# Kernel optimization log

Measured on AMD Instinct MI355X. Metric: run time of the kernel, lower is better.

Reference implementation:

```python
import jax, jax.numpy as jnp
import numpy as np
from jax import lax

N, D, H = 4096, 768, 16384


def setup_inputs() -> dict:
    key = jax.random.key(0)
    k0, k1, k2, k3, k4, k5, k6 = jax.random.split(key, 7)
    bound_e = 1.0 / np.sqrt(D)   # kaiming_uniform(a=sqrt(5)) on (H, D) -> bound 1/sqrt(fan_in)
    bound_d = 1.0 / np.sqrt(H)   # nn.Linear default init, fan_in = H
    return {
        "vision_embeddings": jax.random.normal(k0, (N, D), dtype=jnp.float32),
        "text_embeddings": jax.random.normal(k1, (N, D), dtype=jnp.float32),
        "encoder": jax.random.uniform(k2, (H, D), jnp.float32, -bound_e, bound_e),
        "Wv": jax.random.uniform(k3, (D, H), jnp.float32, -bound_d, bound_d),
        "bv": jax.random.uniform(k4, (D,), jnp.float32, -bound_d, bound_d),
        "Wt": jax.random.uniform(k5, (D, H), jnp.float32, -bound_d, bound_d),
        "bt": jax.random.uniform(k6, (D,), jnp.float32, -bound_d, bound_d),
        "topk": 32,
    }


def _l2norm(x, axis):
    return x / jnp.maximum(jnp.linalg.norm(x, axis=axis, keepdims=True), 1e-12)


def _encode(emb, encoder, topk):
    # F.normalize rows, then cdist(p=2) between unit vectors: ||a-b|| = sqrt(2-2 a.b)
    w = _l2norm(encoder, axis=1)            # [H, D]
    e = _l2norm(emb, axis=1)                # [N, D]
    cos = jnp.einsum("nd,hd->nh", e, w)     # [N, H]
    dist = jnp.sqrt(jnp.maximum(2.0 - 2.0 * cos, 0.0))
    sim = 2.0 - dist                         # [N, H]
    # kthvalue(abs, k=H-topk) == (topk+1)-th largest; keep strictly-greater entries
    abs_f = jnp.abs(sim)
    thres = lax.top_k(abs_f, topk + 1)[0][:, -1]  # [N]
    mask = (abs_f > thres[:, None]).astype(sim.dtype)
    return sim * mask


def reference(vision_embeddings, text_embeddings, encoder, Wv, bv, Wt, bt, topk):
    latent_v = _encode(vision_embeddings, encoder, topk)          # [N, H]
    recon_v = jnp.einsum("nh,dh->nd", latent_v, Wv) + bv          # [N, D]
    latent_t = _encode(text_embeddings, encoder, topk)            # [N, H]
    recon_t = jnp.einsum("nh,dh->nd", latent_t, Wt) + bt          # [N, D]
    return (recon_v, recon_t, latent_v, latent_t)
```

## Files before the change

### kernel.cpp

```cpp
#include <hip/hip_runtime.h>
#include <math.h>


#define N_ROWS 4096
#define D_DIM  768
#define H_DIM  16384
#define M_TOT  8192
#define TOPK   32
#define MARGIN 1e-3f
#define SEL_CAP 40
#define AMB_CAP 64
#define CCAP   512
#define SCAP   24
#define THR_COS 0.08f
#define THR_SIM_GUARD 0.6436f

typedef __attribute__((ext_vector_type(8))) short short8;
typedef __attribute__((ext_vector_type(4))) float floatx4;

__device__ inline unsigned short bf16_rne(float f) {
    unsigned u = __float_as_uint(f);
    unsigned r = u + 0x7fffu + ((u >> 16) & 1u);
    return (unsigned short)(r >> 16);
}

__device__ inline void gload16(const unsigned short* g, unsigned short* l) {
    __builtin_amdgcn_global_load_lds(
        (const __attribute__((address_space(1))) void*)g,
        (__attribute__((address_space(3))) void*)l, 16, 0, 0);
}

__global__ void split_all_kernel(const float* __restrict__ embv,
                                 const float* __restrict__ embt,
                                 const float* __restrict__ enc,
                                 unsigned short* __restrict__ Ahi,
                                 unsigned short* __restrict__ Alo,
                                 unsigned short* __restrict__ Bh,
                                 float* __restrict__ invA,
                                 float* __restrict__ invB,
                                 int* __restrict__ cntflag)
{
    int row = blockIdx.x;
    int tid = threadIdx.x;
    if (row < 64) {
        cntflag[row * 256 + tid] = 0;
    }
    const float* src;
    unsigned short *hi, *lo;
    float* invp;
    if (row < N_ROWS) {
        src = embv + (size_t)row * D_DIM;
        hi = Ahi + (size_t)row * D_DIM; lo = Alo + (size_t)row * D_DIM;
        invp = invA + row;
    } else if (row < 2 * N_ROWS) {
        int r = row - N_ROWS;
        src = embt + (size_t)r * D_DIM;
        hi = Ahi + (size_t)row * D_DIM; lo = Alo + (size_t)row * D_DIM;
        invp = invA + row;
    } else {
        int r = row - 2 * N_ROWS;
        src = enc + (size_t)r * D_DIM;
        hi = Bh + (size_t)r * D_DIM; lo = nullptr;
        invp = invB + r;
    }
    __shared__ float red[4];
    const float4* s4 = reinterpret_cast<const float4*>(src);
    float4 v = make_float4(0.f, 0.f, 0.f, 0.f);
    float ss = 0.f;
    if (tid < 192) {
        v = s4[tid];
        ss = v.x * v.x + v.y * v.y + v.z * v.z + v.w * v.w;
    }
    #pragma unroll
    for (int o = 32; o > 0; o >>= 1) ss += __shfl_down(ss, o);
    int wave = tid >> 6, lane = tid & 63;
    if (lane == 0) red[wave] = ss;
    __syncthreads();
    if (tid == 0) {
        float tot = red[0] + red[1] + red[2];
        red[0] = 1.f / fmaxf(sqrtf(tot), 1e-12f);
    }
    __syncthreads();
    float inv = red[0];
    if (tid == 0) *invp = inv;
    if (tid < 192) {
        float x[4] = {v.x * inv, v.y * inv, v.z * inv, v.w * inv};
        unsigned short hh[4], ll[4];
        #pragma unroll
        for (int t = 0; t < 4; t++) {
            hh[t] = bf16_rne(x[t]);
            float hf = __uint_as_float((unsigned)hh[t] << 16);
            ll[t] = bf16_rne(x[t] - hf);
        }
        ushort4 h4; h4.x = hh[0]; h4.y = hh[1]; h4.z = hh[2]; h4.w = hh[3];
        *reinterpret_cast<ushort4*>(hi + tid * 4) = h4;
        if (lo) {
            ushort4 l4; l4.x = ll[0]; l4.y = ll[1]; l4.z = ll[2]; l4.w = ll[3];
            *reinterpret_cast<ushort4*>(lo + tid * 4) = l4;
        }
    }
}

#define GBK 32
#define NTILE (D_DIM / GBK)

__global__ __launch_bounds__(256, 3)
void gemm_mfma_kernel(const unsigned short* __restrict__ Ahi,
                      const unsigned short* __restrict__ Alo,
                      const unsigned short* __restrict__ Bh,
                      int* __restrict__ cand_cnt,
                      int* __restrict__ cand_idx,
                      float* __restrict__ cand_val)
{
    __shared__ unsigned short sA[2][2][128 * GBK];
    __shared__ unsigned short sB[2][128 * GBK];

    int tid = threadIdx.x;
    int lane = tid & 63;
    int wave = tid >> 6;
    int wr = (wave >> 1) * 64;
    int wc = (wave & 1) * 64;
    int m = lane & 15;
    int q = lane >> 4;

    unsigned nwgx = gridDim.x;
    unsigned lid = blockIdx.y * nwgx + blockIdx.x;
    unsigned cpx = (nwgx * gridDim.y) >> 3;
    unsigned swz = (lid & 7u) * cpx + (lid >> 3);
    int bx = (int)(swz % nwgx);
    int by = (int)(swz / nwgx);

    int row0 = by * 128;
    int col0 = bx * 128;

    int p0 = tid, p1 = tid + 256;
    int r0 = ((p0 >> 5) << 3) | (p0 & 7), q0 = (p0 >> 3) & 3;
    int r1 = ((p1 >> 5) << 3) | (p1 & 7), q1 = (p1 >> 3) & 3;
    size_t aoff0 = (size_t)(row0 + r0) * D_DIM + q0 * 8;
    size_t aoff1 = (size_t)(row0 + r1) * D_DIM + q1 * 8;
    size_t boff0 = (size_t)(col0 + r0) * D_DIM + q0 * 8;
    size_t boff1 = (size_t)(col0 + r1) * D_DIM + q1 * 8;

    int am0 = wr + m;
    int bn0 = wc + m;
    int offA = ((am0 >> 3) << 8) + (q << 6) + ((am0 & 7) << 3);
    int offB = ((bn0 >> 3) << 8) + (q << 6) + ((bn0 & 7) << 3);

    floatx4 acc[4][4];
    #pragma unroll
    for (int i = 0; i < 4; i++)
        #pragma unroll
        for (int j = 0; j < 4; j++)
            acc[i][j] = (floatx4){0.f, 0.f, 0.f, 0.f};

    auto stage = [&](int t, int b) {
        int k0 = t * GBK;
        gload16(Ahi + aoff0 + k0, &sA[b][0][p0 * 8]);
        gload16(Ahi + aoff1 + k0, &sA[b][0][p1 * 8]);
        gload16(Alo + aoff0 + k0, &sA[b][1][p0 * 8]);
        gload16(Alo + aoff1 + k0, &sA[b][1][p1 * 8]);
        gload16(Bh + boff0 + k0, &sB[b][p0 * 8]);
        gload16(Bh + boff1 + k0, &sB[b][p1 * 8]);
    };

    auto compute = [&](int b) {
        short8 fah[4], fal[4], fbv[4];
        #pragma unroll
        for (int i = 0; i < 4; i++) {
            fah[i] = *(const short8*)&sA[b][0][offA + i * 512];
            fal[i] = *(const short8*)&sA[b][1][offA + i * 512];
        }
        #pragma unroll
        for (int j = 0; j < 4; j++)
            fbv[j] = *(const short8*)&sB[b][offB + j * 512];
        __builtin_amdgcn_s_setprio(1);
        #pragma unroll
        for (int j = 0; j < 4; j++) {
            #pragma unroll
            for (int i = 0; i < 4; i++) {
                acc[i][j] = __builtin_amdgcn_mfma_f32_16x16x32_bf16(fah[i], fbv[j], acc[i][j], 0, 0, 0);
                acc[i][j] = __builtin_amdgcn_mfma_f32_16x16x32_bf16(fal[i], fbv[j], acc[i][j], 0, 0, 0);
            }
        }
        __builtin_amdgcn_s_setprio(0);
    };

    stage(0, 0);
    int cur = 0;
    for (int t = 0; t < NTILE - 1; ++t) {
        stage(t + 1, cur ^ 1);
        asm volatile("s_waitcnt vmcnt(6)" ::: "memory");
        __builtin_amdgcn_s_barrier();
        __builtin_amdgcn_sched_barrier(0);
        compute(cur);
        __builtin_amdgcn_sched_barrier(0);
        __builtin_amdgcn_s_barrier();
        cur ^= 1;
    }
    asm volatile("s_waitcnt vmcnt(0)" ::: "memory");
    __builtin_amdgcn_s_barrier();
    __builtin_amdgcn_sched_barrier(0);
    compute(cur);

    __syncthreads();
    int*   s_rcnt = (int*)(&sA[0][0][0]);
    int*   s_ridx = s_rcnt + 128;
    float* s_rval = (float*)(s_ridx + 128 * SCAP);
    if (tid < 128) s_rcnt[tid] = 0;
    __syncthreads();

    #pragma unroll
    for (int i = 0; i < 4; i++) {
        #pragma unroll
        for (int r = 0; r < 4; r++) {
            int lrow = wr + i * 16 + q * 4 + r;
            #pragma unroll
            for (int j = 0; j < 4; j++) {
                float cosv = acc[i][j][r];
                if (cosv >= THR_COS) {
                    int s = atomicAdd(&s_rcnt[lrow], 1);
                    if (s < SCAP) {
                        s_ridx[lrow * SCAP + s] = wc + m + j * 16;
                        s_rval[lrow * SCAP + s] = cosv;
                    }
                }
            }
        }
    }
    __syncthreads();

    if (tid < 128) {
        int c = s_rcnt[tid];
        if (c > 0) {
            int grow = row0 + tid;
            int wcnt = (c > SCAP) ? SCAP : c;
            int addc = (c > SCAP) ? (CCAP + 1) : c;
            int base = atomicAdd(&cand_cnt[grow], addc);
            for (int s2 = 0; s2 < wcnt; ++s2) {
                int slot = base + s2;
                if (slot < CCAP) {
                    cand_idx[(size_t)grow * CCAP + slot] = col0 + s_ridx[tid * SCAP + s2];
                    cand_val[(size_t)grow * CCAP + slot] = s_rval[tid * SCAP + s2];
                }
            }
        }
    }
}

__global__ __launch_bounds__(256)
void cand_select_kernel(const int* __restrict__ cand_cnt,
                        const int* __restrict__ cand_idx,
                        const float* __restrict__ cand_val,
                        float* __restrict__ latent,
                        int* __restrict__ sel_cnt,
                        int* __restrict__ sel_idx,
                        float* __restrict__ sel_val,
                        int* __restrict__ amb_cnt,
                        int* __restrict__ amb_idx,
                        int* __restrict__ flag)
{
    int row = blockIdx.x;
    int tid = threadIdx.x;
    float* v = latent + (size_t)row * H_DIM;

    floatx4* vw = (floatx4*)v;
    floatx4 z = (floatx4){0.f, 0.f, 0.f, 0.f};
    #pragma unroll
    for (int k = 0; k < 16; k++)
        __builtin_nontemporal_store(z, &vw[tid + 256 * k]);

    int cnt = cand_cnt[row];

    __shared__ float sv[CCAP];
    __shared__ int   si[CCAP];
    __shared__ int svstar, skept, samb;

    if (cnt > CCAP || cnt < TOPK + 1) {
        if (tid == 0) { flag[row] = 1; sel_cnt[row] = 0; amb_cnt[row] = 0; }
        return;
    }
    for (int c = tid; c < cnt; c += 256) {
        float cosv = cand_val[(size_t)row * CCAP + c];
        sv[c] = 2.f - sqrtf(fmaxf(2.f - 2.f * cosv, 0.f));
        si[c] = cand_idx[(size_t)row * CCAP + c];
    }
    if (tid == 0) { svstar = 0x7FFFFFFF; skept = 0; samb = 0; }
    __syncthreads();

    for (int c = tid; c < cnt; c += 256) {
        float a = sv[c];
        int g = 0;
        for (int j = 0; j < cnt; j++) {
            float aj = sv[j];
            g += (aj > a || (aj == a && j < c)) ? 1 : 0;
        }
        if (g <= TOPK) atomicMin(&svstar, __float_as_int(a));
    }
    __syncthreads();
    float vs = __int_as_float(svstar);

    if (vs - MARGIN <= THR_SIM_GUARD) {
        if (tid == 0) { flag[row] = 1; sel_cnt[row] = 0; amb_cnt[row] = 0; }
        return;
    }

    for (int c = tid; c < cnt; c += 256) {
        float f = sv[c];
        int idx = si[c];
        if (f > vs + MARGIN) {
            int s = atomicAdd(&skept, 1);
            sel_idx[(size_t)row * SEL_CAP + s] = idx;
            sel_val[(size_t)row * SEL_CAP + s] = f;
            v[idx] = f;
        } else if (f >= vs - MARGIN) {
            int s = atomicAdd(&samb, 1);
            if (s < AMB_CAP) amb_idx[(size_t)row * AMB_CAP + s] = idx;
        }
    }
    __syncthreads();
    if (tid == 0) { sel_cnt[row] = skept; amb_cnt[row] = min(samb, AMB_CAP); }
}

__global__ __launch_bounds__(256)
void finalize_kernel(const int* __restrict__ flag,
                     const float* __restrict__ embv,
                     const float* __restrict__ embt,
                     const float* __restrict__ enc,
                     const float* __restrict__ invA,
                     const float* __restrict__ invB,
                     float* __restrict__ latent,
                     int* __restrict__ sel_cnt,
                     int* __restrict__ sel_idx,
                     float* __restrict__ sel_val,
                     int* __restrict__ amb_cnt,
                     const int* __restrict__ amb_idx)
{
    int row = blockIdx.x;
    int tid = threadIdx.x;
    float* v = latent + (size_t)row * H_DIM;
    const float* src = (row < N_ROWS) ? embv + (size_t)row * D_DIM
                                      : embt + (size_t)(row - N_ROWS) * D_DIM;
    float ia = invA[row];

    __shared__ float ssrc[D_DIM];
    __shared__ unsigned hist[256];
    __shared__ unsigned s_prefix;
    __shared__ int s_k, s_cnt;
    __shared__ float ex[AMB_CAP];
    __shared__ int evs, kc;

    if (flag[row]) {
        for (int d = tid; d < D_DIM; d += 256) ssrc[d] = src[d];
        __syncthreads();
        for (int h = tid; h < H_DIM; h += 256) {
            const float* w = enc + (size_t)h * D_DIM;
            float d = 0.f;
            for (int t = 0; t < D_DIM; t++) d += ssrc[t] * w[t];
            float cosv = d * ia * invB[h];
            v[h] = 2.f - sqrtf(fmaxf(2.f - 2.f * cosv, 0.f));
        }
        __syncthreads();
        int k = TOPK + 1;
        unsigned prefix = 0;
        for (int shift = 24; shift >= 0; shift -= 8) {
            hist[tid] = 0;
            __syncthreads();
            unsigned pmask = (shift == 24) ? 0u : (0xFFFFFFFFu << (shift + 8));
            for (int i = tid; i < H_DIM; i += 256) {
                unsigned u = __float_as_uint(v[i]);
                if ((u & pmask) == prefix)
                    atomicAdd(&hist[(u >> shift) & 255u], 1u);
            }
            __syncthreads();
            if (tid == 0) {
                int c = 0, b = 255;
                for (; b >= 0; b--) {
                    c += (int)hist[b];
                    if (c >= k) break;
                }
                if (b < 0) b = 0;
                s_prefix = prefix | ((unsigned)b << shift);
                s_k = k - (c - (int)hist[b]);
            }
            __syncthreads();
            prefix = s_prefix;
            k = s_k;
            __syncthreads();
        }
        float thres = __uint_as_float(prefix);
        if (tid == 0) s_cnt = 0;
        __syncthreads();
        for (int i = tid; i < H_DIM; i += 256) {
            float x = v[i];
            bool keep = (x > thres);
            v[i] = keep ? x : 0.f;
            if (keep) {
                int slot = atomicAdd(&s_cnt, 1);
                if (slot < SEL_CAP) {
                    sel_idx[(size_t)row * SEL_CAP + slot] = i;
                    sel_val[(size_t)row * SEL_CAP + slot] = x;
                }
            }
        }
        __syncthreads();
        if (tid == 0) {
            sel_cnt[row] = (s_cnt > SEL_CAP) ? SEL_CAP : s_cnt;
            amb_cnt[row] = 0;
        }
        return;
    }

    int s = amb_cnt[row];
    if (s == 0) return;
    int m = sel_cnt[row];
    int need = TOPK - m;
    if (need <= 0) return;
    int wave = tid >> 6, lane = tid & 63;
    for (int a = wave; a < s; a += 4) {
        int h = amb_idx[(size_t)row * AMB_CAP + a];
        const float* w = enc + (size_t)h * D_DIM;
        float d = 0.f;
        for (int t = lane; t < D_DIM; t += 64) d += src[t] * w[t];
        #pragma unroll
        for (int o = 32; o > 0; o >>= 1) d += __shfl_down(d, o);
        if (lane == 0) {
            float cosv = d * ia * invB[h];
            ex[a] = 2.f - sqrtf(fmaxf(2.f - 2.f * cosv, 0.f));
        }
    }
    if (tid == 0) { evs = 0x7FFFFFFF; kc = 0; }
    __syncthreads();
    if (tid < s) {
        float mya = fabsf(ex[tid]);
        int g = 0;
        for (int j = 0; j < s; j++) {
            float aj = fabsf(ex[j]);
            g += (aj > mya || (aj == mya && j < tid)) ? 1 : 0;
        }
        if (g <= need) atomicMin(&evs, __float_as_int(mya));
    }
    __syncthreads();
    float ep = __int_as_float(evs);
    if (tid < s) {
        int idx = amb_idx[(size_t)row * AMB_CAP + tid];
        float e = ex[tid];
        if (fabsf(e) > ep) {
            int sl = atomicAdd(&kc, 1);
            v[idx] = e;
            sel_idx[(size_t)row * SEL_CAP + m + sl] = idx;
            sel_val[(size_t)row * SEL_CAP + m + sl] = e;
        }
    }
    __syncthreads();
    if (tid == 0) sel_cnt[row] = m + kc;
}

__global__ void transpose_kernel(const float* __restrict__ Wv,
                                 const float* __restrict__ Wt,
                                 float* __restrict__ WvT,
                                 float* __restrict__ WtT)
{
    int z = blockIdx.z;
    const float* W = z ? Wt : Wv;
    float* WT = z ? WtT : WvT;
    __shared__ float tile[32][33];
    int tx = threadIdx.x & 31;
    int ty = threadIdx.x >> 5;
    int h0 = blockIdx.x * 32;
    int d0 = blockIdx.y * 32;
    #pragma unroll
    for (int t = 0; t < 4; t++)
        tile[ty + t * 8][tx] = W[(size_t)(d0 + ty + t * 8) * H_DIM + h0 + tx];
    __syncthreads();
    #pragma unroll
    for (int t = 0; t < 4; t++)
        WT[(size_t)(h0 + ty + t * 8) * D_DIM + d0 + tx] = tile[tx][ty + t * 8];
}

__global__ void recon_kernel(const float* __restrict__ Wv_,
                             const float* __restrict__ Wt_,
                             const float* __restrict__ bv,
                             const float* __restrict__ bt,
                             const int* __restrict__ sel_cnt,
                             const int* __restrict__ sel_idx,
                             const float* __restrict__ sel_val,
                             long sh, long sd,
                             float* __restrict__ out)
{
    int n = blockIdx.x;
    int z = blockIdx.y;
    int row = z * N_ROWS + n;
    const float* W = z ? Wt_ : Wv_;
    const float* bias = z ? bt : bv;
    float* o = out + (size_t)z * N_ROWS * D_DIM + (size_t)n * D_DIM;

    __shared__ int s_idx[SEL_CAP];
    __shared__ float s_val[SEL_CAP];
    __shared__ int s_cnt;
    int tid = threadIdx.x;
    if (tid == 0) s_cnt = sel_cnt[row];
    __syncthreads();
    int cnt = s_cnt;
    if (tid < cnt) {
        s_idx[tid] = sel_idx[(size_t)row * SEL_CAP + tid];
        s_val[tid] = sel_val[(size_t)row * SEL_CAP + tid];
    }
    __syncthreads();

    for (int d = tid; d < D_DIM; d += 256) {
        float acc = bias[d];
        for (int j = 0; j < cnt; j++)
            acc += s_val[j] * W[(size_t)s_idx[j] * sh + (size_t)d * sd];
        o[d] = acc;
    }
}

__global__ void row_invnorm_kernel(const float* __restrict__ x,
                                   float* __restrict__ inv, int rows) {
    int row = blockIdx.x * 4 + (threadIdx.x >> 6);
    int lane = threadIdx.x & 63;
    if (row >= rows) return;
    const float4* p = reinterpret_cast<const float4*>(x + (size_t)row * D_DIM);
    float ss = 0.f;
    #pragma unroll
    for (int i = 0; i < 3; i++) {
        float4 v = p[lane + i * 64];
        ss += v.x * v.x + v.y * v.y + v.z * v.z + v.w * v.w;
    }
    #pragma unroll
    for (int off = 32; off > 0; off >>= 1) ss += __shfl_down(ss, off);
    if (lane == 0) inv[row] = 1.f / fmaxf(sqrtf(ss), 1e-12f);
}

#define BM 128
#define BN 128
#define BK 16
__global__ __launch_bounds__(256)
void gemm_sim_kernel(const float* __restrict__ embv,
                     const float* __restrict__ embt,
                     const float* __restrict__ enc,
                     const float* __restrict__ inv_emb,
                     const float* __restrict__ inv_enc,
                     float* __restrict__ latent)
{
    int z = blockIdx.z;
    const float* A = z ? embt : embv;
    const float* invA = inv_emb + z * N_ROWS;
    float* C = latent + (size_t)z * N_ROWS * H_DIM;
    __shared__ float As[BK][BM + 4];
    __shared__ float Bs[BK][BN + 4];
    int tid = threadIdx.x;
    int tx = tid & 15, ty = tid >> 4;
    int row0 = blockIdx.y * BM, col0 = blockIdx.x * BN;
    float acc[8][8];
    #pragma unroll
    for (int i = 0; i < 8; i++)
        #pragma unroll
        for (int j = 0; j < 8; j++) acc[i][j] = 0.f;
    for (int k0 = 0; k0 < D_DIM; k0 += BK) {
        #pragma unroll
        for (int t = 0; t < 2; t++) {
            int idx = t * 256 + tid;
            int r = idx >> 2, c4 = idx & 3;
            float4 va = *reinterpret_cast<const float4*>(
                A + (size_t)(row0 + r) * D_DIM + k0 + c4 * 4);
            As[c4 * 4 + 0][r] = va.x; As[c4 * 4 + 1][r] = va.y;
            As[c4 * 4 + 2][r] = va.z; As[c4 * 4 + 3][r] = va.w;
            float4 vb = *reinterpret_cast<const float4*>(
                enc + (size_t)(col0 + r) * D_DIM + k0 + c4 * 4);
            Bs[c4 * 4 + 0][r] = vb.x; Bs[c4 * 4 + 1][r] = vb.y;
            Bs[c4 * 4 + 2][r] = vb.z; Bs[c4 * 4 + 3][r] = vb.w;
        }
        __syncthreads();
        #pragma unroll
        for (int kk = 0; kk < BK; kk++) {
            float a[8], b[8];
            *reinterpret_cast<float4*>(&a[0]) = *reinterpret_cast<const float4*>(&As[kk][ty * 8]);
            *reinterpret_cast<float4*>(&a[4]) = *reinterpret_cast<const float4*>(&As[kk][ty * 8 + 4]);
            *reinterpret_cast<float4*>(&b[0]) = *reinterpret_cast<const float4*>(&Bs[kk][tx * 8]);
            *reinterpret_cast<float4*>(&b[4]) = *reinterpret_cast<const float4*>(&Bs[kk][tx * 8 + 4]);
            #pragma unroll
            for (int i = 0; i < 8; i++)
                #pragma unroll
                for (int j = 0; j < 8; j++)
                    acc[i][j] = fmaf(a[i], b[j], acc[i][j]);
        }
        __syncthreads();
    }
    #pragma unroll
    for (int i = 0; i < 8; i++) {
        int n = row0 + ty * 8 + i;
        float sa = invA[n];
        float* Crow = C + (size_t)n * H_DIM + col0 + tx * 8;
        float tmp[8];
        #pragma unroll
        for (int j = 0; j < 8; j++) {
            float cosv = acc[i][j] * sa * inv_enc[col0 + tx * 8 + j];
            tmp[j] = 2.f - sqrtf(fmaxf(2.f - 2.f * cosv, 0.f));
        }
        float4 o0 = {tmp[0], tmp[1], tmp[2], tmp[3]};
        float4 o1 = {tmp[4], tmp[5], tmp[6], tmp[7]};
        *reinterpret_cast<float4*>(Crow) = o0;
        *reinterpret_cast<float4*>(Crow + 4) = o1;
    }
}

__global__ void legacy_select_kernel(float* __restrict__ latent,
                                     const int* __restrict__ topk_p,
                                     int* __restrict__ sel_cnt,
                                     int* __restrict__ sel_idx,
                                     float* __restrict__ sel_val)
{
    int row = blockIdx.x;
    float* v = latent + (size_t)row * H_DIM;
    int tid = threadIdx.x;
    __shared__ unsigned hist[256];
    __shared__ unsigned s_prefix;
    __shared__ int s_k;
    __shared__ int s_cnt;
    int k = topk_p[0] + 1;
    unsigned prefix = 0;
    for (int shift = 24; shift >= 0; shift -= 8) {
        hist[tid] = 0;
        __syncthreads();
        unsigned pmask = (shift == 24) ? 0u : (0xFFFFFFFFu << (shift + 8));
        for (int i = tid; i < H_DIM; i += 256) {
            unsigned u = __float_as_uint(v[i]) & 0x7FFFFFFFu;
            if ((u & pmask) == prefix)
                atomicAdd(&hist[(u >> shift) & 255u], 1u);
        }
        __syncthreads();
        if (tid == 0) {
            int c = 0, b = 255;
            for (; b >= 0; b--) {
                c += (int)hist[b];
                if (c >= k) break;
            }
            if (b < 0) b = 0;
            s_prefix = prefix | ((unsigned)b << shift);
            s_k = k - (c - (int)hist[b]);
        }
        __syncthreads();
        prefix = s_prefix;
        k = s_k;
        __syncthreads();
    }
    float thres = __uint_as_float(prefix);
    if (tid == 0) s_cnt = 0;
    __syncthreads();
    for (int i = tid; i < H_DIM; i += 256) {
        float x = v[i];
        bool keep = (fabsf(x) > thres);
        v[i] = keep ? x : 0.f;
        if (keep) {
            int slot = atomicAdd(&s_cnt, 1);
            if (slot < SEL_CAP) {
                sel_idx[(size_t)row * SEL_CAP + slot] = i;
                sel_val[(size_t)row * SEL_CAP + slot] = x;
            }
        }
    }
    __syncthreads();
    if (tid == 0) sel_cnt[row] = (s_cnt > SEL_CAP) ? SEL_CAP : s_cnt;
}

extern "C" void kernel_launch(void* const* d_in, const int* in_sizes, int n_in,
                              void* d_out, int out_size, void* d_ws, size_t ws_size,
                              hipStream_t stream) {
    const float* embv = (const float*)d_in[0];
    const float* embt = (const float*)d_in[1];
    const float* enc  = (const float*)d_in[2];
    const float* Wv   = (const float*)d_in[3];
    const float* bv   = (const float*)d_in[4];
    const float* Wt   = (const float*)d_in[5];
    const float* bt   = (const float*)d_in[6];
    const int* topk   = (const int*)d_in[7];
    float* out = (float*)d_out;

    float* recon_out = out;
    float* latent = out + (size_t)2 * N_ROWS * D_DIM;

    char* ws = (char*)d_ws;
    size_t off = 0;
    float* invA = (float*)(ws + off);            off += (size_t)M_TOT * 4;
    float* invB = (float*)(ws + off);            off += (size_t)H_DIM * 4;
    int*   sel_cnt = (int*)(ws + off);           off += (size_t)M_TOT * 4;
    int*   amb_cnt = (int*)(ws + off);           off += (size_t)M_TOT * 4;
    int*   sel_idx = (int*)(ws + off);           off += (size_t)M_TOT * SEL_CAP * 4;
    float* sel_val = (float*)(ws + off);         off += (size_t)M_TOT * SEL_CAP * 4;
    int*   amb_idx = (int*)(ws + off);           off += (size_t)M_TOT * AMB_CAP * 4;
    int*   cand_cnt = (int*)(ws + off);          off += (size_t)M_TOT * 4;
    int*   flag     = (int*)(ws + off);          off += (size_t)M_TOT * 4;
    unsigned short* Ahi = (unsigned short*)(ws + off); off += (size_t)M_TOT * D_DIM * 2;
    unsigned short* Alo = (unsigned short*)(ws + off); off += (size_t)M_TOT * D_DIM * 2;
    unsigned short* Bh  = (unsigned short*)(ws + off); off += (size_t)H_DIM * D_DIM * 2;
    size_t core_need = off;

    int*   cand_idx = (int*)(ws + off);
    float* cand_val = (float*)(ws + off + (size_t)M_TOT * CCAP * 4);
    size_t cand_bytes = (size_t)M_TOT * CCAP * 8;
    float* WvT = (float*)(ws + off);
    float* WtT = WvT + (size_t)D_DIM * H_DIM;
    size_t trans_bytes = (size_t)2 * D_DIM * H_DIM * 4;

    if (ws_size >= core_need + cand_bytes) {
        bool use_T = ws_size >= core_need + trans_bytes;

        split_all_kernel<<<2 * N_ROWS + H_DIM, 256, 0, stream>>>(
            embv, embt, enc, Ahi, Alo, Bh, invA, invB, cand_cnt);

        gemm_mfma_kernel<<<dim3(H_DIM / 128, M_TOT / 128), 256, 0, stream>>>(
            Ahi, Alo, Bh, cand_cnt, cand_idx, cand_val);

        cand_select_kernel<<<M_TOT, 256, 0, stream>>>(
            cand_cnt, cand_idx, cand_val, latent,
            sel_cnt, sel_idx, sel_val, amb_cnt, amb_idx, flag);

        finalize_kernel<<<M_TOT, 256, 0, stream>>>(
            flag, embv, embt, enc, invA, invB, latent,
            sel_cnt, sel_idx, sel_val, amb_cnt, amb_idx);

        if (use_T) {
            transpose_kernel<<<dim3(H_DIM / 32, D_DIM / 32, 2), 256, 0, stream>>>(
                Wv, Wt, WvT, WtT);
            recon_kernel<<<dim3(N_ROWS, 2), 256, 0, stream>>>(
                WvT, WtT, bv, bt, sel_cnt, sel_idx, sel_val, (long)D_DIM, 1L, recon_out);
        } else {
            recon_kernel<<<dim3(N_ROWS, 2), 256, 0, stream>>>(
                Wv, Wt, bv, bt, sel_cnt, sel_idx, sel_val, 1L, (long)H_DIM, recon_out);
        }
    } else {
        size_t o2 = 0;
        float* inv_enc = (float*)(ws + o2); o2 += (size_t)H_DIM * 4;
        float* inv_emb = (float*)(ws + o2); o2 += (size_t)2 * N_ROWS * 4;
        int*   l_cnt = (int*)(ws + o2);     o2 += (size_t)2 * N_ROWS * 4;
        int*   l_idx = (int*)(ws + o2);     o2 += (size_t)2 * N_ROWS * SEL_CAP * 4;
        float* l_val = (float*)(ws + o2);   o2 += (size_t)2 * N_ROWS * SEL_CAP * 4;
        row_invnorm_kernel<<<H_DIM / 4, 256, 0, stream>>>(enc, inv_enc, H_DIM);
        row_invnorm_kernel<<<N_ROWS / 4, 256, 0, stream>>>(embv, inv_emb, N_ROWS);
        row_invnorm_kernel<<<N_ROWS / 4, 256, 0, stream>>>(embt, inv_emb + N_ROWS, N_ROWS);
        dim3 g(H_DIM / BN, N_ROWS / BM, 2);
        gemm_sim_kernel<<<g, 256, 0, stream>>>(embv, embt, enc, inv_emb, inv_enc, latent);
        legacy_select_kernel<<<2 * N_ROWS, 256, 0, stream>>>(latent, topk, l_cnt, l_idx, l_val);
        recon_kernel<<<dim3(N_ROWS, 2), 256, 0, stream>>>(
            Wv, Wt, bv, bt, l_cnt, l_idx, l_val, 1L, (long)H_DIM, recon_out);
    }
}
```

Measured before the change: 1.454 ms.

## Fuse candidate selection with finalize and add vectorized float4 recon kernel

Merges the candidate-select and finalize kernels into one per-row kernel, so ambiguous indices stay in shared memory and the flag, amb_cnt and amb_idx round trips through global memory plus one launch are removed. The fallback dot product now uses float4 loads. Reconstruction uses a new 192-thread kernel where each thread accumulates a float4 slice of the transposed weights. The host also drops the non-transposed path and requires workspace for the transposed weights. Fusing the two kernels may raise shared-memory use and register pressure in the combined kernel.

```diff
diff --git a/kernel.cpp b/kernel.cpp
--- a/kernel.cpp
+++ b/kernel.cpp
@@ -248,16 +248,18 @@
 }
 
 __global__ __launch_bounds__(256)
-void cand_select_kernel(const int* __restrict__ cand_cnt,
-                        const int* __restrict__ cand_idx,
-                        const float* __restrict__ cand_val,
-                        float* __restrict__ latent,
-                        int* __restrict__ sel_cnt,
-                        int* __restrict__ sel_idx,
-                        float* __restrict__ sel_val,
-                        int* __restrict__ amb_cnt,
-                        int* __restrict__ amb_idx,
-                        int* __restrict__ flag)
+void select_finalize_kernel(const int* __restrict__ cand_cnt,
+                            const int* __restrict__ cand_idx,
+                            const float* __restrict__ cand_val,
+                            const float* __restrict__ embv,
+                            const float* __restrict__ embt,
+                            const float* __restrict__ enc,
+                            const float* __restrict__ invA,
+                            const float* __restrict__ invB,
+                            float* __restrict__ latent,
+                            int* __restrict__ sel_cnt,
+                            int* __restrict__ sel_idx,
+                            float* __restrict__ sel_val)
 {
     int row = blockIdx.x;
     int tid = threadIdx.x;
@@ -273,34 +275,100 @@
 
     __shared__ float sv[CCAP];
     __shared__ int   si[CCAP];
-    __shared__ int svstar, skept, samb;
-
-    if (cnt > CCAP || cnt < TOPK + 1) {
-        if (tid == 0) { flag[row] = 1; sel_cnt[row] = 0; amb_cnt[row] = 0; }
-        return;
-    }
-    for (int c = tid; c < cnt; c += 256) {
-        float cosv = cand_val[(size_t)row * CCAP + c];
-        sv[c] = 2.f - sqrtf(fmaxf(2.f - 2.f * cosv, 0.f));
-        si[c] = cand_idx[(size_t)row * CCAP + c];
-    }
-    if (tid == 0) { svstar = 0x7FFFFFFF; skept = 0; samb = 0; }
-    __syncthreads();
-
-    for (int c = tid; c < cnt; c += 256) {
-        float a = sv[c];
-        int g = 0;
-        for (int j = 0; j < cnt; j++) {
-            float aj = sv[j];
-            g += (aj > a || (aj == a && j < c)) ? 1 : 0;
-        }
-        if (g <= TOPK) atomicMin(&svstar, __float_as_int(a));
-    }
-    __syncthreads();
-    float vs = __int_as_float(svstar);
-
-    if (vs - MARGIN <= THR_SIM_GUARD) {
-        if (tid == 0) { flag[row] = 1; sel_cnt[row] = 0; amb_cnt[row] = 0; }
+    __shared__ int   s_amb[AMB_CAP];
+    __shared__ float ex[AMB_CAP];
+    __shared__ float ssrc[D_DIM];
+    __shared__ unsigned hist[256];
+    __shared__ unsigned s_prefix;
+    __shared__ int svstar, skept, samb, s_k, s_cnt2, evs, kc;
+
+    bool bad = (cnt > CCAP || cnt < TOPK + 1);
+    float vs = 0.f;
+    if (!bad) {
+        for (int c = tid; c < cnt; c += 256) {
+            float cosv = cand_val[(size_t)row * CCAP + c];
+            sv[c] = 2.f - sqrtf(fmaxf(2.f - 2.f * cosv, 0.f));
+            si[c] = cand_idx[(size_t)row * CCAP + c];
+        }
+        if (tid == 0) { svstar = 0x7FFFFFFF; skept = 0; samb = 0; }
+        __syncthreads();
+        for (int c = tid; c < cnt; c += 256) {
+            float a = sv[c];
+            int g = 0;
+            for (int j = 0; j < cnt; j++) {
+                float aj = sv[j];
+                g += (aj > a || (aj == a && j < c)) ? 1 : 0;
+            }
+            if (g <= TOPK) atomicMin(&svstar, __float_as_int(a));
+        }
+        __syncthreads();
+        vs = __int_as_float(svstar);
+        bad = (vs - MARGIN <= THR_SIM_GUARD);
+    }
+
+    const float* src = (row < N_ROWS) ? embv + (size_t)row * D_DIM
+                                      : embt + (size_t)(row - N_ROWS) * D_DIM;
+    float ia = invA[row];
+
+    if (bad) {
+        for (int d = tid; d < D_DIM; d += 256) ssrc[d] = src[d];
+        __syncthreads();
+        const floatx4* s4 = (const floatx4*)ssrc;
+        for (int h = tid; h < H_DIM; h += 256) {
+            const floatx4* w4 = (const floatx4*)(enc + (size_t)h * D_DIM);
+            float d = 0.f;
+            for (int t = 0; t < D_DIM / 4; t++) {
+                floatx4 a = s4[t], b = w4[t];
+                d += a.x * b.x + a.y * b.y + a.z * b.z + a.w * b.w;
+            }
+            float cosv = d * ia * invB[h];
+            v[h] = 2.f - sqrtf(fmaxf(2.f - 2.f * cosv, 0.f));
+        }
+        __syncthreads();
+        int k = TOPK + 1;
+        unsigned prefix = 0;
+        for (int shift = 24; shift >= 0; shift -= 8) {
+            hist[tid] = 0;
+            __syncthreads();
+            unsigned pmask = (shift == 24) ? 0u : (0xFFFFFFFFu << (shift + 8));
+            for (int i = tid; i < H_DIM; i += 256) {
+                unsigned u = __float_as_uint(v[i]);
+                if ((u & pmask) == prefix)
+                    atomicAdd(&hist[(u >> shift) & 255u], 1u);
+            }
+            __syncthreads();
+            if (tid == 0) {
+                int c = 0, b = 255;
+                for (; b >= 0; b--) {
+                    c += (int)hist[b];
+                    if (c >= k) break;
+                }
+                if (b < 0) b = 0;
+                s_prefix = prefix | ((unsigned)b << shift);
+                s_k = k - (c - (int)hist[b]);
+            }
+            __syncthreads();
+            prefix = s_prefix;
+            k = s_k;
+            __syncthreads();
+        }
+        float thres = __uint_as_float(prefix);
+        if (tid == 0) s_cnt2 = 0;
+        __syncthreads();
+        for (int i = tid; i < H_DIM; i += 256) {
+            float x = v[i];
+            bool keep = (x > thres);
+            v[i] = keep ? x : 0.f;
+            if (keep) {
+                int slot = atomicAdd(&s_cnt2, 1);
+                if (slot < SEL_CAP) {
+                    sel_idx[(size_t)row * SEL_CAP + slot] = i;
+                    sel_val[(size_t)row * SEL_CAP + slot] = x;
+                }
+            }
+        }
+        __syncthreads();
+        if (tid == 0) sel_cnt[row] = (s_cnt2 > SEL_CAP) ? SEL_CAP : s_cnt2;
         return;
     }
 
@@ -314,110 +382,21 @@
             v[idx] = f;
         } else if (f >= vs - MARGIN) {
             int s = atomicAdd(&samb, 1);
-            if (s < AMB_CAP) amb_idx[(size_t)row * AMB_CAP + s] = idx;
-        }
-    }
-    __syncthreads();
-    if (tid == 0) { sel_cnt[row] = skept; amb_cnt[row] = min(samb, AMB_CAP); }
-}
-
-__global__ __launch_bounds__(256)
-void finalize_kernel(const int* __restrict__ flag,
-                     const float* __restrict__ embv,
-                     const float* __restrict__ embt,
-                     const float* __restrict__ enc,
-                     const float* __restrict__ invA,
-                     const float* __restrict__ invB,
-                     float* __restrict__ latent,
-                     int* __restrict__ sel_cnt,
-                     int* __restrict__ sel_idx,
-                     float* __restrict__ sel_val,
-                     int* __restrict__ amb_cnt,
-                     const int* __restrict__ amb_idx)
-{
-    int row = blockIdx.x;
-    int tid = threadIdx.x;
-    float* v = latent + (size_t)row * H_DIM;
-    const float* src = (row < N_ROWS) ? embv + (size_t)row * D_DIM
-                                      : embt + (size_t)(row - N_ROWS) * D_DIM;
-    float ia = invA[row];
-
-    __shared__ float ssrc[D_DIM];
-    __shared__ unsigned hist[256];
-    __shared__ unsigned s_prefix;
-    __shared__ int s_k, s_cnt;
-    __shared__ float ex[AMB_CAP];
-    __shared__ int evs, kc;
-
-    if (flag[row]) {
-        for (int d = tid; d < D_DIM; d += 256) ssrc[d] = src[d];
-        __syncthreads();
-        for (int h = tid; h < H_DIM; h += 256) {
-            const float* w = enc + (size_t)h * D_DIM;
-            float d = 0.f;
-            for (int t = 0; t < D_DIM; t++) d += ssrc[t] * w[t];
-            float cosv = d * ia * invB[h];
-            v[h] = 2.f - sqrtf(fmaxf(2.f - 2.f * cosv, 0.f));
-        }
-        __syncthreads();
-        int k = TOPK + 1;
-        unsigned prefix = 0;
-        for (int shift = 24; shift >= 0; shift -= 8) {
-            hist[tid] = 0;
-            __syncthreads();
-            unsigned pmask = (shift == 24) ? 0u : (0xFFFFFFFFu << (shift + 8));
-            for (int i = tid; i < H_DIM; i += 256) {
-                unsigned u = __float_as_uint(v[i]);
-                if ((u & pmask) == prefix)
-                    atomicAdd(&hist[(u >> shift) & 255u], 1u);
-            }
-            __syncthreads();
-            if (tid == 0) {
-                int c = 0, b = 255;
-                for (; b >= 0; b--) {
-                    c += (int)hist[b];
-                    if (c >= k) break;
-                }
-                if (b < 0) b = 0;
-                s_prefix = prefix | ((unsigned)b << shift);
-                s_k = k - (c - (int)hist[b]);
-            }
-            __syncthreads();
-            prefix = s_prefix;
-            k = s_k;
-            __syncthreads();
-        }
-        float thres = __uint_as_float(prefix);
-        if (tid == 0) s_cnt = 0;
-        __syncthreads();
-        for (int i = tid; i < H_DIM; i += 256) {
-            float x = v[i];
-            bool keep = (x > thres);
-            v[i] = keep ? x : 0.f;
-            if (keep) {
-                int slot = atomicAdd(&s_cnt, 1);
-                if (slot < SEL_CAP) {
-                    sel_idx[(size_t)row * SEL_CAP + slot] = i;
-                    sel_val[(size_t)row * SEL_CAP + slot] = x;
-                }
-            }
-        }
-        __syncthreads();
-        if (tid == 0) {
-            sel_cnt[row] = (s_cnt > SEL_CAP) ? SEL_CAP : s_cnt;
-            amb_cnt[row] = 0;
-        }
+            if (s < AMB_CAP) s_amb[s] = idx;
+        }
+    }
+    __syncthreads();
+    int m_ = skept;
+    int s_ = min(samb, AMB_CAP);
+    int need = TOPK - m_;
+    if (s_ == 0 || need <= 0) {
+        if (tid == 0) sel_cnt[row] = m_;
         return;
     }
 
-    int s = amb_cnt[row];
-    if (s == 0) return;
-    int m = sel_cnt[row];
-    int need = TOPK - m;
-    if (need <= 0) return;
     int wave = tid >> 6, lane = tid & 63;
-    for (int a = wave; a < s; a += 4) {
-        int h = amb_idx[(size_t)row * AMB_CAP + a];
+    for (int a = wave; a < s_; a += 4) {
+        int h = s_amb[a];
         const float* w = enc + (size_t)h * D_DIM;
         float d = 0.f;
         for (int t = lane; t < D_DIM; t += 64) d += src[t] * w[t];
@@ -430,10 +409,10 @@
     }
     if (tid == 0) { evs = 0x7FFFFFFF; kc = 0; }
     __syncthreads();
-    if (tid < s) {
+    if (tid < s_) {
         float mya = fabsf(ex[tid]);
         int g = 0;
-        for (int j = 0; j < s; j++) {
+        for (int j = 0; j < s_; j++) {
             float aj = fabsf(ex[j]);
             g += (aj > mya || (aj == mya && j < tid)) ? 1 : 0;
         }
@@ -441,18 +420,18 @@
     }
     __syncthreads();
     float ep = __int_as_float(evs);
-    if (tid < s) {
-        int idx = amb_idx[(size_t)row * AMB_CAP + tid];
+    if (tid < s_) {
+        int idx = s_amb[tid];
         float e = ex[tid];
         if (fabsf(e) > ep) {
             int sl = atomicAdd(&kc, 1);
             v[idx] = e;
-            sel_idx[(size_t)row * SEL_CAP + m + sl] = idx;
-            sel_val[(size_t)row * SEL_CAP + m + sl] = e;
-        }
-    }
-    __syncthreads();
-    if (tid == 0) sel_cnt[row] = m + kc;
+            sel_idx[(size_t)row * SEL_CAP + m_ + sl] = idx;
+            sel_val[(size_t)row * SEL_CAP + m_ + sl] = e;
+        }
+    }
+    __syncthreads();
+    if (tid == 0) sel_cnt[row] = m_ + kc;
 }
 
 __global__ void transpose_kernel(const float* __restrict__ Wv,
@@ -475,6 +454,46 @@
     #pragma unroll
     for (int t = 0; t < 4; t++)
         WT[(size_t)(h0 + ty + t * 8) * D_DIM + d0 + tx] = tile[tx][ty + t * 8];
+}
+
+__global__ __launch_bounds__(192)
+void recon4_kernel(const float* __restrict__ WvT,
+                   const float* __restrict__ WtT,
+                   const float* __restrict__ bv,
+                   const float* __restrict__ bt,
+                   const int* __restrict__ sel_cnt,
+                   const int* __restrict__ sel_idx,
+                   const float* __restrict__ sel_val,
+                   float* __restrict__ out)
+{
+    int n = blockIdx.x;
+    int z = blockIdx.y;
+    int row = z * N_ROWS + n;
+    const float* W = z ? WtT : WvT;
+    const float* bias = z ? bt : bv;
+    float* o = out + (size_t)z * N_ROWS * D_DIM + (size_t)n * D_DIM;
+
+    __shared__ int s_idx[SEL_CAP];
+    __shared__ float s_val[SEL_CAP];
+    __shared__ int s_cnt;
+    int tid = threadIdx.x;
+    if (tid == 0) s_cnt = sel_cnt[row];
+    __syncthreads();
+    int cnt = s_cnt;
+    if (tid < cnt) {
+        s_idx[tid] = sel_idx[(size_t)row * SEL_CAP + tid];
+        s_val[tid] = sel_val[(size_t)row * SEL_CAP + tid];
+    }
+    __syncthreads();
+
+    float4 acc = reinterpret_cast<const float4*>(bias)[tid];
+    for (int j = 0; j < cnt; j++) {
+        float4 w = reinterpret_cast<const float4*>(W + (size_t)s_idx[j] * D_DIM)[tid];
+        float vv = s_val[j];
+        acc.x += vv * w.x; acc.y += vv * w.y;
+        acc.z += vv * w.z; acc.w += vv * w.w;
+    }
+    reinterpret_cast<float4*>(o)[tid] = acc;
 }
 
 __global__ void recon_kernel(const float* __restrict__ Wv_,
@@ -695,6 +714,7 @@
     unsigned short* Alo = (unsigned short*)(ws + off); off += (size_t)M_TOT * D_DIM * 2;
     unsigned short* Bh  = (unsigned short*)(ws + off); off += (size_t)H_DIM * D_DIM * 2;
     size_t core_need = off;
+    (void)amb_cnt; (void)amb_idx; (void)flag;
 
     int*   cand_idx = (int*)(ws + off);
     float* cand_val = (float*)(ws + off + (size_t)M_TOT * CCAP * 4);
@@ -702,33 +722,24 @@
     float* WvT = (float*)(ws + off);
     float* WtT = WvT + (size_t)D_DIM * H_DIM;
     size_t trans_bytes = (size_t)2 * D_DIM * H_DIM * 4;
-
-    if (ws_size >= core_need + cand_bytes) {
-        bool use_T = ws_size >= core_need + trans_bytes;
-
+    (void)cand_bytes;
+
+    if (ws_size >= core_need + trans_bytes) {
         split_all_kernel<<<2 * N_ROWS + H_DIM, 256, 0, stream>>>(
             embv, embt, enc, Ahi, Alo, Bh, invA, invB, cand_cnt);
 
         gemm_mfma_kernel<<<dim3(H_DIM / 128, M_TOT / 128), 256, 0, stream>>>(
             Ahi, Alo, Bh, cand_cnt, cand_idx, cand_val);
 
-        cand_select_kernel<<<M_TOT, 256, 0, stream>>>(
-            cand_cnt, cand_idx, cand_val, latent,
-            sel_cnt, sel_idx, sel_val, amb_cnt, amb_idx, flag);
-
-        finalize_kernel<<<M_TOT, 256, 0, stream>>>(
-            flag, embv, embt, enc, invA, invB, latent,
-            sel_cnt, sel_idx, sel_val, amb_cnt, amb_idx);
-
-        if (use_T) {
-            transpose_kernel<<<dim3(H_DIM / 32, D_DIM / 32, 2), 256, 0, stream>>>(
-                Wv, Wt, WvT, WtT);
-            recon_kernel<<<dim3(N_ROWS, 2), 256, 0, stream>>>(
-                WvT, WtT, bv, bt, sel_cnt, sel_idx, sel_val, (long)D_DIM, 1L, recon_out);
-        } else {
-            recon_kernel<<<dim3(N_ROWS, 2), 256, 0, stream>>>(
-                Wv, Wt, bv, bt, sel_cnt, sel_idx, sel_val, 1L, (long)H_DIM, recon_out);
-        }
+        select_finalize_kernel<<<M_TOT, 256, 0, stream>>>(
+            cand_cnt, cand_idx, cand_val, embv, embt, enc, invA, invB,
+            latent, sel_cnt, sel_idx, sel_val);
+
+        transpose_kernel<<<dim3(H_DIM / 32, D_DIM / 32, 2), 256, 0, stream>>>(
+            Wv, Wt, WvT, WtT);
+
+        recon4_kernel<<<dim3(N_ROWS, 2), 192, 0, stream>>>(
+            WvT, WtT, bv, bt, sel_cnt, sel_idx, sel_val, recon_out);
     } else {
         size_t o2 = 0;
         float* inv_enc = (float*)(ws + o2); o2 += (size_t)H_DIM * 4;
```

Result: faster. 1.420 ms (-2.3%).
